# Optimization experiments

Hardware: AMD Instinct MI355X
Metric: run time of the kernel (lower is better)

The kernel has to match this reference:

```python
import jax, jax.numpy as jnp
import numpy as np

K = 4096          # in_features
N = 11008         # out_features
GROUP = 128       # scale group size along K
PACK = 16
BATCH, SEQ = 2, 4096


def setup_inputs() -> dict:
    key = jax.random.key(0)
    k1, k2, k3, k4 = jax.random.split(key, 4)
    x = jax.random.normal(k1, (BATCH, SEQ, K), dtype=jnp.float16)
    # valid ternary codes in {0,1,2} encoding w = code - 1 in {-1,0,+1}
    codes = jax.random.randint(k2, (K, N), 0, 3, dtype=jnp.int32)
    codes = codes.reshape(K // PACK, PACK, N)
    shifts = (2 * jnp.arange(PACK, dtype=jnp.int32))[None, :, None]
    packed_weight = jnp.sum(codes << shifts, axis=1).astype(jnp.int32)  # (K//16, N)
    scales = (jax.random.uniform(k3, (K // GROUP, N), dtype=jnp.float32) * 0.1 + 0.01).astype(jnp.float16)
    bias = (jax.random.normal(k4, (N,), dtype=jnp.float32) * 0.01).astype(jnp.float16)
    return {"x": x, "packed_weight": packed_weight, "scales": scales, "bias": bias}


def _dequant(packed_weight, scales):
    # unpack 16 two-bit codes per int32 along K
    shifts = (2 * jnp.arange(PACK, dtype=jnp.int32))[None, :, None]
    codes = (packed_weight[:, None, :] >> shifts) & 3        # (K//16, 16, N)
    Kp = packed_weight.shape[0] * PACK
    Nn = packed_weight.shape[1]
    w = (codes.astype(jnp.float16) - jnp.float16(1.0)).reshape(Kp, Nn)  # ternary {-1,0,1}
    scale_full = jnp.repeat(scales, GROUP, axis=0)            # (K, N) group-wise gamma
    return w * scale_full


def reference(x, packed_weight, scales, bias):
    Kp = packed_weight.shape[0] * PACK
    Nn = packed_weight.shape[1]
    w = _dequant(packed_weight, scales)                       # (K, N) fp16
    x2 = x.reshape(-1, Kp).astype(jnp.float16)                # (M, K)
    out = jnp.dot(x2, w, preferred_element_type=jnp.float32).astype(jnp.float16)
    out = out + bias
    return out.reshape(*x.shape[:-1], Nn)
```

## Files before the change

kernel.cpp:

```cpp
#include <hip/hip_runtime.h>
#include <stdint.h>

#define K_DIM 4096
#define N_DIM 11008
#define M_DIM 8192
#define BM 256
#define BN 256
#define BK 64
#define NSLAB (K_DIM / BK)
#define ABUF (BM * BK)
#define BBUF (BN * BK)
#define NWG ((N_DIM / BN) * (M_DIM / BM))

#define FBM 128
#define FBK 32
#define FASTRIDE 32
#define FBSTRIDE 40

typedef _Float16 half8  __attribute__((ext_vector_type(8)));
typedef _Float16 half2v __attribute__((ext_vector_type(2)));
typedef float    floatx4 __attribute__((ext_vector_type(4)));

#define WS_NEEDED ((size_t)M_DIM * K_DIM * 2)

__device__ __forceinline__ void async_lds16(const void* g, void* l) {
    __builtin_amdgcn_global_load_lds(
        (const __attribute__((address_space(1))) uint32_t*)g,
        (__attribute__((address_space(3))) uint32_t*)l, 16, 0, 0);
}

__global__ __launch_bounds__(256) void cvt_a(const float* __restrict__ x,
                                             _Float16* __restrict__ xh) {
    const size_t i = ((size_t)blockIdx.x * 256 + threadIdx.x) * 8;
    const float4 a = *(const float4*)(x + i);
    const float4 b = *(const float4*)(x + i + 4);
    half8 h;
    h[0] = (_Float16)a.x; h[1] = (_Float16)a.y; h[2] = (_Float16)a.z; h[3] = (_Float16)a.w;
    h[4] = (_Float16)b.x; h[5] = (_Float16)b.y; h[6] = (_Float16)b.z; h[7] = (_Float16)b.w;
    *(half8*)(xh + i) = h;
}

__global__ __launch_bounds__(512, 2) void ternary_gemm_db(
    const _Float16* __restrict__ xh,
    const int*   __restrict__ pw,
    const float* __restrict__ scales,
    const float* __restrict__ bias,
    float*       __restrict__ out)
{
    __shared__ __align__(16) _Float16 lds_a[2 * ABUF];
    __shared__ __align__(16) _Float16 lds_b[2 * BBUF];

    const int tid  = threadIdx.x;
    const int lane = tid & 63;
    const int w    = tid >> 6;

    const int bid = blockIdx.x;
    const int swz = (bid & 7) * (NWG / 8) + (bid >> 3);
    const int n0 = (swz % (N_DIM / BN)) * BN;
    const int m0 = (swz / (N_DIM / BN)) * BM;

    const int band = (w & 3) * 64;
    const int wn   = (w >> 2) * 128;

    const int arow = lane >> 3;
    const int achk = (lane & 7) ^ arow;
    const _Float16* gaBase = xh + (size_t)(m0 + band + arow) * K_DIM + achk * 8;

    const int nb = tid >> 1;
    const int kp = tid & 1;
    const int* pwp = pw + (size_t)(kp * 2) * N_DIM + n0 + nb;
    const float* scp = scales + n0 + nb;
    const int s7  = nb & 7;
    const int c0a = ((kp * 2 + 0) * 2 + 0) ^ s7;
    const int c0b = ((kp * 2 + 0) * 2 + 1) ^ s7;
    const int c1a = ((kp * 2 + 1) * 2 + 0) ^ s7;
    const int c1b = ((kp * 2 + 1) * 2 + 1) ^ s7;

    floatx4 acc[4][8];
    #pragma unroll
    for (int i = 0; i < 4; ++i)
        #pragma unroll
        for (int j = 0; j < 8; ++j)
            acc[i][j] = floatx4{0.f, 0.f, 0.f, 0.f};

    const int lr = lane & 15;
    const int g  = lane >> 4;
    const int x7 = lr & 7;

    int aoff[4], boff[8];
    #pragma unroll
    for (int mt = 0; mt < 4; ++mt) aoff[mt] = (band + mt * 16 + lr) * BK;
    #pragma unroll
    for (int nt = 0; nt < 8; ++nt) boff[nt] = (wn + nt * 16 + lr) * BK;

    auto permq = [](uint32_t v, uint32_t tmpl, uint32_t* q) {
        #pragma unroll
        for (int j = 0; j < 8; ++j) {
            uint32_t t4 = (v >> (4 * j)) & 0xFu;
            uint32_t sp = (t4 | (t4 << 14)) & 0x00030003u;
            uint32_t sel = ((sp & 0x00010001u) << 1) | ((0x00030003u - sp) << 8);
            q[j] = __builtin_amdgcn_perm(tmpl, tmpl, sel);
        }
    };
    auto stage_b = [&](uint32_t v0, uint32_t v1, float scf, _Float16* rowb) {
        _Float16 sh = (_Float16)scf;
        uint32_t sbits = (uint32_t)__builtin_bit_cast(unsigned short, sh);
        uint32_t tmpl = sbits | (((sbits >> 8) ^ 0x80u) << 24);
        uint32_t q[8];
        permq(v0, tmpl, q);
        *(uint4*)(rowb + c0a * 8) = make_uint4(q[0], q[1], q[2], q[3]);
        *(uint4*)(rowb + c0b * 8) = make_uint4(q[4], q[5], q[6], q[7]);
        permq(v1, tmpl, q);
        *(uint4*)(rowb + c1a * 8) = make_uint4(q[0], q[1], q[2], q[3]);
        *(uint4*)(rowb + c1b * 8) = make_uint4(q[4], q[5], q[6], q[7]);
    };
    auto stage_a = [&](int slab, int buf) {
        const _Float16* gk = gaBase + slab * BK;
        _Float16* dst = lds_a + buf * ABUF + band * BK;
        #pragma unroll
        for (int i = 0; i < 8; ++i)
            async_lds16(gk + (size_t)i * 8 * K_DIM, dst + i * 8 * BK);
    };

    uint32_t pv00 = (uint32_t)pwp[0];
    uint32_t pv01 = (uint32_t)pwp[(size_t)1 * N_DIM];
    float    sc0  = scp[0];
    uint32_t pvA0 = (uint32_t)pwp[(size_t)4 * N_DIM];
    uint32_t pvA1 = (uint32_t)pwp[(size_t)5 * N_DIM];
    float    scA  = scp[0];
    stage_a(0, 0);
    stage_b(pv00, pv01, sc0, lds_b + nb * BK);
    asm volatile("s_waitcnt lgkmcnt(0)" ::: "memory");
    __builtin_amdgcn_s_barrier();

    uint32_t pvB0 = 0, pvB1 = 0; float scB = 0.f;

    for (int t = 0; t < NSLAB; ++t) {
        const int cur = t & 1;

        if (t + 2 < NSLAB) {
            pvB0 = (uint32_t)pwp[(size_t)((t + 2) * 4 + 0) * N_DIM];
            pvB1 = (uint32_t)pwp[(size_t)((t + 2) * 4 + 1) * N_DIM];
            scB  = scp[(size_t)((t + 2) >> 1) * N_DIM];
        }
        if (t + 1 < NSLAB) {
            stage_a(t + 1, cur ^ 1);
            stage_b(pvA0, pvA1, scA, lds_b + (cur ^ 1) * BBUF + nb * BK);
        }

        if (t + 2 < NSLAB)      asm volatile("s_waitcnt vmcnt(11)" ::: "memory");
        else if (t + 1 < NSLAB) asm volatile("s_waitcnt vmcnt(8)"  ::: "memory");
        else                    asm volatile("s_waitcnt vmcnt(0)"  ::: "memory");

        const _Float16* Ab = lds_a + cur * ABUF;
        const _Float16* Bb = lds_b + cur * BBUF;
        __builtin_amdgcn_s_setprio(1);
        #pragma unroll
        for (int h = 0; h < 2; ++h) {
            const int co = ((h * 4 + g) ^ x7) * 8;
            half8 af[4], bf[8];
            #pragma unroll
            for (int mt = 0; mt < 4; ++mt) af[mt] = *(const half8*)&Ab[aoff[mt] + co];
            #pragma unroll
            for (int nt = 0; nt < 8; ++nt) bf[nt] = *(const half8*)&Bb[boff[nt] + co];
            #pragma unroll
            for (int mt = 0; mt < 4; ++mt)
                #pragma unroll
                for (int nt = 0; nt < 8; ++nt)
                    acc[mt][nt] = __builtin_amdgcn_mfma_f32_16x16x32_f16(
                        af[mt], bf[nt], acc[mt][nt], 0, 0, 0);
        }
        __builtin_amdgcn_s_setprio(0);

        if (t + 1 < NSLAB) {
            asm volatile("s_waitcnt lgkmcnt(0)" ::: "memory");
            __builtin_amdgcn_s_barrier();
        }
        pvA0 = pvB0; pvA1 = pvB1; scA = scB;
    }

    float bv[8];
    #pragma unroll
    for (int nt = 0; nt < 8; ++nt) bv[nt] = bias[n0 + wn + nt * 16 + lr];

    const int rbase = g * 4;
    #pragma unroll
    for (int mt = 0; mt < 4; ++mt) {
        #pragma unroll
        for (int nt = 0; nt < 8; ++nt) {
            const int col = n0 + wn + nt * 16 + lr;
            float* op = out + (size_t)(m0 + band + mt * 16 + rbase) * N_DIM + col;
            floatx4 a = acc[mt][nt];
            #pragma unroll
            for (int r = 0; r < 4; ++r)
                op[(size_t)r * N_DIM] = a[r] + bv[nt];
        }
    }
}

__global__ __launch_bounds__(256, 2) void ternary_gemm(
    const float* __restrict__ x,
    const int*   __restrict__ pw,
    const float* __restrict__ scales,
    const float* __restrict__ bias,
    float*       __restrict__ out)
{
    __shared__ __align__(16) _Float16 lds_a[FBM * FASTRIDE];
    __shared__ __align__(16) _Float16 lds_b[FBM * FBSTRIDE];

    const int tid  = threadIdx.x;
    const int lane = tid & 63;
    const int wave = tid >> 6;

    const int n0 = blockIdx.x * FBM;
    const int m0 = blockIdx.y * FBM;

    const int wm = (wave & 1) * 64;
    const int wn = (wave >> 1) * 64;

    const int nb  = tid & 127;
    const int kpi = tid >> 7;
    const int*   pwp = pw + (size_t)kpi * N_DIM + n0 + nb;
    const float* scp = scales + n0 + nb;
    _Float16* bl = lds_b + nb * FBSTRIDE + kpi * 16;

    floatx4 acc[4][4];
    #pragma unroll
    for (int i = 0; i < 4; ++i)
        #pragma unroll
        for (int j = 0; j < 4; ++j)
            acc[i][j] = floatx4{0.f, 0.f, 0.f, 0.f};

    const int lr = lane & 15;
    const int qk = (lane >> 4) * 8;

    for (int slab = 0; slab < K_DIM / FBK; ++slab) {
        const int k0 = slab * FBK;

        #pragma unroll
        for (int i = 0; i < 4; ++i) {
            const int idx = tid + i * 256;
            const int row = idx >> 3;
            const int kq  = (idx & 7) * 4;
            float4 v4 = *(const float4*)(x + (size_t)(m0 + row) * K_DIM + k0 + kq);
            half2v h0; h0[0] = (_Float16)v4.x; h0[1] = (_Float16)v4.y;
            half2v h1; h1[0] = (_Float16)v4.z; h1[1] = (_Float16)v4.w;
            *(uint2*)(lds_a + row * FASTRIDE + kq) =
                make_uint2(__builtin_bit_cast(uint32_t, h0),
                           __builtin_bit_cast(uint32_t, h1));
        }

        uint32_t v  = (uint32_t)pwp[(size_t)slab * 2 * N_DIM];
        _Float16 sh = (_Float16)scp[(size_t)(slab >> 2) * N_DIM];
        uint32_t sbits = (uint32_t)__builtin_bit_cast(unsigned short, sh);
        uint32_t tmpl = sbits | (((sbits >> 8) ^ 0x80u) << 24);

        uint32_t q[8];
        #pragma unroll
        for (int j = 0; j < 8; ++j) {
            uint32_t t4 = (v >> (4 * j)) & 0xFu;
            uint32_t sp = (t4 | (t4 << 14)) & 0x00030003u;
            uint32_t sel = ((sp & 0x00010001u) << 1) | ((0x00030003u - sp) << 8);
            q[j] = __builtin_amdgcn_perm(tmpl, tmpl, sel);
        }
        *(uint4*)(bl)     = make_uint4(q[0], q[1], q[2], q[3]);
        *(uint4*)(bl + 8) = make_uint4(q[4], q[5], q[6], q[7]);

        __syncthreads();

        half8 af[4], bfr[4];
        #pragma unroll
        for (int t = 0; t < 4; ++t) {
            af[t]  = *(const half8*)&lds_a[(wm + t * 16 + lr) * FASTRIDE + qk];
            bfr[t] = *(const half8*)&lds_b[(wn + t * 16 + lr) * FBSTRIDE + qk];
        }
        #pragma unroll
        for (int mt = 0; mt < 4; ++mt)
            #pragma unroll
            for (int nt = 0; nt < 4; ++nt)
                acc[mt][nt] = __builtin_amdgcn_mfma_f32_16x16x32_f16(
                    af[mt], bfr[nt], acc[mt][nt], 0, 0, 0);

        __syncthreads();
    }

    float bv[4];
    #pragma unroll
    for (int nt = 0; nt < 4; ++nt) bv[nt] = bias[n0 + wn + nt * 16 + lr];

    const int rbase = (lane >> 4) * 4;
    #pragma unroll
    for (int mt = 0; mt < 4; ++mt) {
        #pragma unroll
        for (int nt = 0; nt < 4; ++nt) {
            const int col = n0 + wn + nt * 16 + lr;
            float* op = out + (size_t)(m0 + wm + mt * 16 + rbase) * N_DIM + col;
            floatx4 a = acc[mt][nt];
            #pragma unroll
            for (int r = 0; r < 4; ++r)
                op[(size_t)r * N_DIM] = a[r] + bv[nt];
        }
    }
}

extern "C" void kernel_launch(void* const* d_in, const int* in_sizes, int n_in,
                              void* d_out, int out_size, void* d_ws, size_t ws_size,
                              hipStream_t stream) {
    const float* x  = (const float*)d_in[0];
    const int*   pw = (const int*)d_in[1];
    const float* sc = (const float*)d_in[2];
    const float* bs = (const float*)d_in[3];
    float* out = (float*)d_out;

    if (d_ws != nullptr && ws_size >= WS_NEEDED) {
        _Float16* xh = (_Float16*)d_ws;
        cvt_a<<<dim3((unsigned)((size_t)M_DIM * K_DIM / (256 * 8))), 256, 0, stream>>>(x, xh);
        ternary_gemm_db<<<dim3(NWG), 512, 0, stream>>>(xh, pw, sc, bs, out);
    } else {
        ternary_gemm<<<dim3(N_DIM / FBM, M_DIM / FBM), 256, 0, stream>>>(x, pw, sc, bs, out);
    }
}
```

Baseline: 1.269 ms.

## Restructure ternary GEMM main loop into eight-phase interleaved schedule

The wave layout changes from 4x2 to 2x4 (each wave now covers 128 rows by 64 columns), and each K-slab is split into four quarter MFMA blocks. Between the quarters the kernel interleaves LDS fragment loads, half-slab async A staging, packed-weight prefetch and B dequantisation, separated by workgroup barriers. The aim is to hide global-load and dequant latency behind MFMA work in a ping-pong style. The cost is many more barriers per slab, and a tighter vmcnt wait that relies on the exact count of outstanding loads.

```diff
diff --git a/kernel.cpp b/kernel.cpp
--- a/kernel.cpp
+++ b/kernel.cpp
@@ -10,7 +10,8 @@
 #define NSLAB (K_DIM / BK)
 #define ABUF (BM * BK)
 #define BBUF (BN * BK)
-#define NWG ((N_DIM / BN) * (M_DIM / BM))
+#define NBN (N_DIM / BN)
+#define NWG (NBN * (M_DIM / BM))
 
 #define FBM 128
 #define FBK 32
@@ -40,7 +41,7 @@
     *(half8*)(xh + i) = h;
 }
 
-__global__ __launch_bounds__(512, 2) void ternary_gemm_db(
+__global__ __launch_bounds__(512, 2) void ternary_gemm_8p(
     const _Float16* __restrict__ xh,
     const int*   __restrict__ pw,
     const float* __restrict__ scales,
@@ -56,15 +57,22 @@
 
     const int bid = blockIdx.x;
     const int swz = (bid & 7) * (NWG / 8) + (bid >> 3);
-    const int n0 = (swz % (N_DIM / BN)) * BN;
-    const int m0 = (swz / (N_DIM / BN)) * BM;
-
-    const int band = (w & 3) * 64;
-    const int wn   = (w >> 2) * 128;
-
-    const int arow = lane >> 3;
-    const int achk = (lane & 7) ^ arow;
-    const _Float16* gaBase = xh + (size_t)(m0 + band + arow) * K_DIM + achk * 8;
+    const int n0 = (swz % NBN) * BN;
+    const int m0 = (swz / NBN) * BM;
+
+    const int wm = (w >> 2) * 128;
+    const int wn = (w & 3) * 64;
+
+    const _Float16* gaS[4];
+    int laOff[4];
+    #pragma unroll
+    for (int r = 0; r < 4; ++r) {
+        const int idx = tid + r * 512;
+        const int row = idx >> 3;
+        const int c   = idx & 7;
+        gaS[r]   = xh + (size_t)(m0 + row) * K_DIM + ((c ^ (row & 7)) * 8);
+        laOff[r] = idx * 8;
+    }
 
     const int nb = tid >> 1;
     const int kp = tid & 1;
@@ -75,23 +83,18 @@
     const int c0b = ((kp * 2 + 0) * 2 + 1) ^ s7;
     const int c1a = ((kp * 2 + 1) * 2 + 0) ^ s7;
     const int c1b = ((kp * 2 + 1) * 2 + 1) ^ s7;
-
-    floatx4 acc[4][8];
-    #pragma unroll
-    for (int i = 0; i < 4; ++i)
-        #pragma unroll
-        for (int j = 0; j < 8; ++j)
+    const int blOff = nb * BK;
+
+    floatx4 acc[8][4];
+    #pragma unroll
+    for (int i = 0; i < 8; ++i)
+        #pragma unroll
+        for (int j = 0; j < 4; ++j)
             acc[i][j] = floatx4{0.f, 0.f, 0.f, 0.f};
 
     const int lr = lane & 15;
     const int g  = lane >> 4;
     const int x7 = lr & 7;
-
-    int aoff[4], boff[8];
-    #pragma unroll
-    for (int mt = 0; mt < 4; ++mt) aoff[mt] = (band + mt * 16 + lr) * BK;
-    #pragma unroll
-    for (int nt = 0; nt < 8; ++nt) boff[nt] = (wn + nt * 16 + lr) * BK;
 
     auto permq = [](uint32_t v, uint32_t tmpl, uint32_t* q) {
         #pragma unroll
@@ -102,7 +105,8 @@
             q[j] = __builtin_amdgcn_perm(tmpl, tmpl, sel);
         }
     };
-    auto stage_b = [&](uint32_t v0, uint32_t v1, float scf, _Float16* rowb) {
+    auto stage_b = [&](uint32_t v0, uint32_t v1, float scf, int buf) {
+        _Float16* rowb = lds_b + buf * BBUF + blOff;
         _Float16 sh = (_Float16)scf;
         uint32_t sbits = (uint32_t)__builtin_bit_cast(unsigned short, sh);
         uint32_t tmpl = sbits | (((sbits >> 8) ^ 0x80u) << 24);
@@ -114,86 +118,115 @@
         *(uint4*)(rowb + c1a * 8) = make_uint4(q[0], q[1], q[2], q[3]);
         *(uint4*)(rowb + c1b * 8) = make_uint4(q[4], q[5], q[6], q[7]);
     };
-    auto stage_a = [&](int slab, int buf) {
-        const _Float16* gk = gaBase + slab * BK;
-        _Float16* dst = lds_a + buf * ABUF + band * BK;
-        #pragma unroll
-        for (int i = 0; i < 8; ++i)
-            async_lds16(gk + (size_t)i * 8 * K_DIM, dst + i * 8 * BK);
-    };
-
-    uint32_t pv00 = (uint32_t)pwp[0];
-    uint32_t pv01 = (uint32_t)pwp[(size_t)1 * N_DIM];
-    float    sc0  = scp[0];
+    auto stage_a_h = [&](int t, int buf, int h) {
+        #pragma unroll
+        for (int r = 2 * h; r < 2 * h + 2; ++r)
+            async_lds16(gaS[r] + t * BK, lds_a + buf * ABUF + laOff[r]);
+    };
+    auto ldA = [&](const _Float16* Ab, int q, half8* af) {
+        #pragma unroll
+        for (int mt = 0; mt < 4; ++mt)
+            #pragma unroll
+            for (int ks = 0; ks < 2; ++ks)
+                af[mt * 2 + ks] = *(const half8*)
+                    &Ab[(wm + q * 64 + mt * 16 + lr) * BK + (((ks * 4 + g) ^ x7) * 8)];
+    };
+    auto ldB = [&](const _Float16* Bb, int rr, half8* bf) {
+        #pragma unroll
+        for (int nt = 0; nt < 2; ++nt)
+            #pragma unroll
+            for (int ks = 0; ks < 2; ++ks)
+                bf[nt * 2 + ks] = *(const half8*)
+                    &Bb[(wn + rr * 32 + nt * 16 + lr) * BK + (((ks * 4 + g) ^ x7) * 8)];
+    };
+    auto MM = [&](int q, int rr, const half8* af, const half8* bf) {
+        __builtin_amdgcn_s_setprio(1);
+        #pragma unroll
+        for (int ks = 0; ks < 2; ++ks)
+            #pragma unroll
+            for (int mt = 0; mt < 4; ++mt)
+                #pragma unroll
+                for (int nt = 0; nt < 2; ++nt)
+                    acc[q * 4 + mt][rr * 2 + nt] = __builtin_amdgcn_mfma_f32_16x16x32_f16(
+                        af[mt * 2 + ks], bf[nt * 2 + ks], acc[q * 4 + mt][rr * 2 + nt], 0, 0, 0);
+        __builtin_amdgcn_s_setprio(0);
+    };
+
+    {
+        uint32_t p0 = (uint32_t)pwp[0];
+        uint32_t p1 = (uint32_t)pwp[(size_t)1 * N_DIM];
+        float s0 = scp[0];
+        stage_a_h(0, 0, 0); stage_a_h(0, 0, 1);
+        stage_b(p0, p1, s0, 0);
+    }
     uint32_t pvA0 = (uint32_t)pwp[(size_t)4 * N_DIM];
     uint32_t pvA1 = (uint32_t)pwp[(size_t)5 * N_DIM];
     float    scA  = scp[0];
-    stage_a(0, 0);
-    stage_b(pv00, pv01, sc0, lds_b + nb * BK);
-    asm volatile("s_waitcnt lgkmcnt(0)" ::: "memory");
+    asm volatile("s_waitcnt vmcnt(0) lgkmcnt(0)" ::: "memory");
     __builtin_amdgcn_s_barrier();
 
     uint32_t pvB0 = 0, pvB1 = 0; float scB = 0.f;
 
     for (int t = 0; t < NSLAB; ++t) {
         const int cur = t & 1;
-
-        if (t + 2 < NSLAB) {
+        const _Float16* Ab = lds_a + cur * ABUF;
+        const _Float16* Bb = lds_b + cur * BBUF;
+        const bool stg  = (t + 1 < NSLAB);
+        const bool pref = (t + 2 < NSLAB);
+
+        half8 af[8], bf0[4], bf1[4];
+
+        ldA(Ab, 0, af);
+        ldB(Bb, 0, bf0);
+        if (stg) stage_a_h(t + 1, cur ^ 1, 0);
+        __builtin_amdgcn_s_barrier();
+        MM(0, 0, af, bf0);
+        __builtin_amdgcn_s_barrier();
+
+        ldB(Bb, 1, bf1);
+        if (stg) stage_a_h(t + 1, cur ^ 1, 1);
+        __builtin_amdgcn_s_barrier();
+        MM(0, 1, af, bf1);
+        __builtin_amdgcn_s_barrier();
+
+        ldA(Ab, 1, af);
+        if (pref) {
             pvB0 = (uint32_t)pwp[(size_t)((t + 2) * 4 + 0) * N_DIM];
             pvB1 = (uint32_t)pwp[(size_t)((t + 2) * 4 + 1) * N_DIM];
             scB  = scp[(size_t)((t + 2) >> 1) * N_DIM];
         }
-        if (t + 1 < NSLAB) {
-            stage_a(t + 1, cur ^ 1);
-            stage_b(pvA0, pvA1, scA, lds_b + (cur ^ 1) * BBUF + nb * BK);
-        }
-
-        if (t + 2 < NSLAB)      asm volatile("s_waitcnt vmcnt(11)" ::: "memory");
-        else if (t + 1 < NSLAB) asm volatile("s_waitcnt vmcnt(8)"  ::: "memory");
-        else                    asm volatile("s_waitcnt vmcnt(0)"  ::: "memory");
-
-        const _Float16* Ab = lds_a + cur * ABUF;
-        const _Float16* Bb = lds_b + cur * BBUF;
-        __builtin_amdgcn_s_setprio(1);
-        #pragma unroll
-        for (int h = 0; h < 2; ++h) {
-            const int co = ((h * 4 + g) ^ x7) * 8;
-            half8 af[4], bf[8];
-            #pragma unroll
-            for (int mt = 0; mt < 4; ++mt) af[mt] = *(const half8*)&Ab[aoff[mt] + co];
-            #pragma unroll
-            for (int nt = 0; nt < 8; ++nt) bf[nt] = *(const half8*)&Bb[boff[nt] + co];
-            #pragma unroll
-            for (int mt = 0; mt < 4; ++mt)
-                #pragma unroll
-                for (int nt = 0; nt < 8; ++nt)
-                    acc[mt][nt] = __builtin_amdgcn_mfma_f32_16x16x32_f16(
-                        af[mt], bf[nt], acc[mt][nt], 0, 0, 0);
-        }
-        __builtin_amdgcn_s_setprio(0);
-
-        if (t + 1 < NSLAB) {
+        __builtin_amdgcn_s_barrier();
+        MM(1, 1, af, bf1);
+        __builtin_amdgcn_s_barrier();
+
+        if (stg) {
+            stage_b(pvA0, pvA1, scA, cur ^ 1);
+            if (pref) asm volatile("s_waitcnt vmcnt(2)" ::: "memory");
+            else      asm volatile("s_waitcnt vmcnt(0)" ::: "memory");
             asm volatile("s_waitcnt lgkmcnt(0)" ::: "memory");
-            __builtin_amdgcn_s_barrier();
-        }
+        }
+        __builtin_amdgcn_s_barrier();
+        MM(1, 0, af, bf0);
+        __builtin_amdgcn_s_barrier();
+
         pvA0 = pvB0; pvA1 = pvB1; scA = scB;
     }
 
-    float bv[8];
-    #pragma unroll
-    for (int nt = 0; nt < 8; ++nt) bv[nt] = bias[n0 + wn + nt * 16 + lr];
+    float bv[4];
+    #pragma unroll
+    for (int nt = 0; nt < 4; ++nt) bv[nt] = bias[n0 + wn + nt * 16 + lr];
 
     const int rbase = g * 4;
     #pragma unroll
-    for (int mt = 0; mt < 4; ++mt) {
-        #pragma unroll
-        for (int nt = 0; nt < 8; ++nt) {
-            const int col = n0 + wn + nt * 16 + lr;
-            float* op = out + (size_t)(m0 + band + mt * 16 + rbase) * N_DIM + col;
-            floatx4 a = acc[mt][nt];
+    for (int i = 0; i < 8; ++i) {
+        #pragma unroll
+        for (int j = 0; j < 4; ++j) {
+            const int col = n0 + wn + j * 16 + lr;
+            float* op = out + (size_t)(m0 + wm + i * 16 + rbase) * N_DIM + col;
+            floatx4 a = acc[i][j];
             #pragma unroll
             for (int r = 0; r < 4; ++r)
-                op[(size_t)r * N_DIM] = a[r] + bv[nt];
+                op[(size_t)r * N_DIM] = a[r] + bv[j];
         }
     }
 }
@@ -315,7 +348,7 @@
     if (d_ws != nullptr && ws_size >= WS_NEEDED) {
         _Float16* xh = (_Float16*)d_ws;
         cvt_a<<<dim3((unsigned)((size_t)M_DIM * K_DIM / (256 * 8))), 256, 0, stream>>>(x, xh);
-        ternary_gemm_db<<<dim3(NWG), 512, 0, stream>>>(xh, pw, sc, bs, out);
+        ternary_gemm_8p<<<dim3(NWG), 512, 0, stream>>>(xh, pw, sc, bs, out);
     } else {
         ternary_gemm<<<dim3(N_DIM / FBM, M_DIM / FBM), 256, 0, stream>>>(x, pw, sc, bs, out);
     }
```

Result: slower. 1.414 ms (+11.4%).
